# Kernel tuning notes

Measured on AMD Instinct MI355X. Metric: run time of the kernel, lower is better.

The kernel has to match this reference:

```python
import jax, jax.numpy as jnp
import numpy as np

B, C, H, W = 8, 4, 96, 96
HW = H * W
PCT = 95.0            # TRUNCATED_HAUSDORFF_PERCENTILE
IGNORE = 0            # HD_IGNORE_CLASS_INDEX


def setup_inputs() -> dict:
    key = jax.random.key(0)
    k1, k2 = jax.random.split(key)
    predictions = jax.random.normal(k1, (B, C, H, W), dtype=jnp.float32)
    labels = jax.random.randint(k2, (B, H, W), 0, C, dtype=jnp.int32)
    return {"predictions": predictions, "labels": labels}


def _masked_percentile(vals, mask, q):
    """np.percentile(vals[mask], q) with linear interpolation; invalid -> +inf sort to end."""
    n = jnp.sum(mask)
    s = jnp.sort(jnp.where(mask, vals, jnp.inf))
    pos = (q / 100.0) * jnp.maximum(n - 1, 0).astype(vals.dtype)
    lo = jnp.floor(pos).astype(jnp.int32)
    hi = jnp.ceil(pos).astype(jnp.int32)
    frac = pos - lo.astype(vals.dtype)
    return s[lo] * (1.0 - frac) + s[hi] * frac


def _hausdorff(predictions, labels):
    # argmax of softmax == argmax of logits, but keep the softmax for faithfulness
    pred_cls = jnp.argmax(jax.nn.softmax(predictions, axis=1), axis=1)  # [B,H,W]
    cls_ids = jnp.arange(C)
    mask_a = (pred_cls[:, None] == cls_ids[None, :, None, None]).reshape(B * C, HW)  # pred one-hot
    mask_b = (labels[:, None] == cls_ids[None, :, None, None]).reshape(B * C, HW)    # label one-hot

    # Pixel coordinates (row, col) as in np.argwhere; pairwise Euclidean distances once.
    ys, xs = jnp.meshgrid(jnp.arange(H), jnp.arange(W), indexing="ij")
    coords = jnp.stack([ys.ravel(), xs.ravel()], axis=1).astype(jnp.float32)  # [HW,2]
    sq = jnp.sum(coords * coords, axis=1)
    D = jnp.sqrt(jnp.maximum(sq[:, None] + sq[None, :] - 2.0 * (coords @ coords.T), 0.0))  # [HW,HW]

    def per_pair(masks):
        ma, mb = masks  # [HW] bool each
        fwd_min = jnp.min(jnp.where(mb[None, :], D, jnp.inf), axis=1)  # min dist A-pixel -> B set
        rev_min = jnp.min(jnp.where(ma[:, None], D, jnp.inf), axis=0)  # min dist B-pixel -> A set
        f = _masked_percentile(fwd_min, ma, PCT)
        r = _masked_percentile(rev_min, mb, PCT)
        return jnp.stack([f, r, jnp.maximum(f, r)])

    res = jax.lax.map(per_pair, (mask_a, mask_b)).reshape(B, C, 3)
    valid = (jnp.arange(C) != IGNORE)
    per_class = jnp.where(valid[None, :, None], res, 0.0).mean(axis=0)  # [C,3] mean over batch

    def finalize(v):  # v: [C] -> [C+2]: per-class, mean(all), mean(excluding class 0)
        return jnp.concatenate([v, jnp.mean(v)[None], jnp.mean(v[1:])[None]])

    FHD = finalize(per_class[:, 0])
    RHD = finalize(per_class[:, 1])
    MHD = finalize(per_class[:, 2])
    return MHD, FHD, RHD


def reference(predictions, labels):
    return _hausdorff(predictions, labels)
```

## Files before the change

kernel.cpp:

```cpp
#include <hip/hip_runtime.h>
#include <math.h>

#define B_   8
#define C_   4
#define H_   96
#define W_   96
#define HW_  9216
#define NBINS 18052
#define INFBIN 18051
#define NH32 ((NBINS + 1) / 2)
#define NT   1024
#define NBLK 64
#define NW   16

__global__ __launch_bounds__(NT) void hd_main(const float* __restrict__ preds,
                                              const int*   __restrict__ labels,
                                              float* __restrict__ frws)
{
    __shared__ unsigned long long qmask[HW_ / 64];
    __shared__ unsigned long long tmask[HW_ / 64];
    __shared__ unsigned short g2u[HW_];
    __shared__ unsigned int   h32[NH32];
    __shared__ int wsum[NW];
    __shared__ int twv[NW], qwv[NW], zwv[NW], bwv[NW];
    __shared__ int svsel[2];

    const int id  = blockIdx.x;
    const int dir = id & 1;
    const int bc  = id >> 1;
    const int b   = bc >> 2;
    const int c   = bc & 3;
    const int tid = threadIdx.x;
    const int lane = tid & 63;
    const int wid  = tid >> 6;

    const float* Pb = preds  + (size_t)b * C_ * HW_;
    const int*   Lb = labels + (size_t)b * HW_;

    for (int i = tid; i < NH32; i += NT) h32[i] = 0u;
    if (tid == 0) { svsel[0] = -1; svsel[1] = -1; }

    {
        int myT = 0, myQ = 0, myN0 = 0;
        #pragma unroll 3
        for (int k = 0; k < HW_ / NT; ++k) {
            const int p = k * NT + tid;
            float v0 = Pb[p];
            float v1 = Pb[HW_ + p];
            float v2 = Pb[2 * HW_ + p];
            float v3 = Pb[3 * HW_ + p];
            int bi = 0; float bv = v0;
            if (v1 > bv) { bv = v1; bi = 1; }
            if (v2 > bv) { bv = v2; bi = 2; }
            if (v3 > bv) { bv = v3; bi = 3; }
            const int lab = Lb[p];
            const bool pm = (bi == c);
            const bool lm = (lab == c);
            const bool qm = dir ? lm : pm;
            const bool tm = dir ? pm : lm;
            const unsigned long long qb = __ballot(qm);
            const unsigned long long tb = __ballot(tm);
            if (lane == 0) {
                qmask[p >> 6] = qb;
                tmask[p >> 6] = tb;
                myQ  += __popcll(qb);
                myT  += __popcll(tb);
                myN0 += __popcll(qb & tb);
            }
        }
        if (lane == 0) { twv[wid] = myT; qwv[wid] = myQ; zwv[wid] = myN0; }
    }
    __syncthreads();

    int nT = 0;
    #pragma unroll
    for (int w = 0; w < NW; ++w) nT += twv[w];
    const int tEmpty = (nT == 0);

    for (int k = 0; k < HW_ / NT; ++k) {
        const int p = k * NT + tid;
        const int y = p / W_;
        const int x = p - y * W_;
        const int bp = y * W_;
        const int wi = bp >> 6;
        const int sh = bp & 63;
        const unsigned long long w0 = tmask[wi];
        const unsigned long long w1 = tmask[wi + 1];
        unsigned long long A, Bw;
        if (sh == 0) { A = w0;                       Bw = w1 & 0xFFFFFFFFull; }
        else         { A = (w0 >> 32) | (w1 << 32); Bw = w1 >> 32; }

        int dl = 1000, dr = 1000;
        if (x < 64) {
            const unsigned long long ml = A & ((2ull << x) - 1ull);
            if (ml) dl = x - (63 - __builtin_clzll(ml));
            const unsigned long long mr = A & ~((1ull << x) - 1ull);
            if (mr)      dr = __builtin_ctzll(mr) - x;
            else if (Bw) dr = 64 + __builtin_ctzll(Bw) - x;
        } else {
            const int xb = x - 64;
            const unsigned long long ml = Bw & ((2ull << xb) - 1ull);
            if (ml)     dl = x - (64 + 63 - __builtin_clzll(ml));
            else if (A) dl = x - (63 - __builtin_clzll(A));
            const unsigned long long mr = Bw & ~((1ull << xb) - 1ull);
            if (mr) dr = 64 + __builtin_ctzll(mr) - x;
        }
        const int g = min(dl, dr);
        g2u[p] = (g >= 96) ? (unsigned short)40000
                           : (unsigned short)(g * g);
    }
    __syncthreads();

    {
        int bmax = 0;
        if (!tEmpty) {
            for (int k = 0; k < HW_ / NT; ++k) {
                const int p = k * NT + tid;
                const int qbit = (int)((qmask[p >> 6] >> (p & 63)) & 1ull);
                if (!qbit) continue;
                const int tbit = (int)((tmask[p >> 6] >> (p & 63)) & 1ull);
                if (tbit) continue;
                const int y = p / W_;
                const int x = p - y * W_;
                const int a0 = (int)g2u[p];
                const int a1 = (y >= 1)      ? (int)g2u[p - W_]     : 0x7FFF0000;
                const int a2 = (y + 1 < H_)  ? (int)g2u[p + W_]     : 0x7FFF0000;
                const int a3 = (y >= 2)      ? (int)g2u[p - 2 * W_] : 0x7FFF0000;
                const int a4 = (y + 2 < H_)  ? (int)g2u[p + 2 * W_] : 0x7FFF0000;
                int best = min(a0, min(min(a1 + 1, a2 + 1), min(a3 + 4, a4 + 4)));
                for (int off = 3; off < H_; ++off) {
                    const int o2 = off * off;
                    if (o2 >= best) break;
                    const int r1 = y - off;
                    const int r2 = y + off;
                    if (r1 >= 0) best = min(best, o2 + (int)g2u[r1 * W_ + x]);
                    if (r2 < H_) best = min(best, o2 + (int)g2u[r2 * W_ + x]);
                }
                bmax = max(bmax, best);
                atomicAdd(&h32[best >> 1], 1u << ((best & 1) << 4));
            }
        }
        #pragma unroll
        for (int d = 32; d >= 1; d >>= 1) bmax = max(bmax, __shfl_xor(bmax, d, 64));
        if (lane == 0) bwv[wid] = bmax;
    }
    __syncthreads();

    int nQ = 0, n0 = 0, maxd2 = 0;
    #pragma unroll
    for (int w = 0; w < NW; ++w) {
        nQ += qwv[w]; n0 += zwv[w]; maxd2 = max(maxd2, bwv[w]);
    }
    const int h0x = (!tEmpty) ? n0 : 0;
    const int CHUNK = (NBINS + NT - 1) / NT;
    const int base_i = tid * CHUNK;
    int lsum = (base_i == 0) ? h0x : 0;
    for (int j = 0; j < CHUNK; ++j) {
        const int i = base_i + j;
        if (i > maxd2) break;
        lsum += (int)((h32[i >> 1] >> ((i & 1) << 4)) & 0xFFFFu);
    }
    int incl = lsum;
    #pragma unroll
    for (int d = 1; d < 64; d <<= 1) {
        const int t = __shfl_up(incl, d, 64);
        if (lane >= d) incl += t;
    }
    if (lane == 63) wsum[wid] = incl;
    __syncthreads();
    if (wid == 0) {
        const int w = (lane < NW) ? wsum[lane] : 0;
        int wincl = w;
        #pragma unroll
        for (int d = 1; d < NW; d <<= 1) {
            const int t = __shfl_up(wincl, d, 64);
            if (lane >= d) wincl += t;
        }
        if (lane < NW) wsum[lane] = wincl - w;
    }
    __syncthreads();

    int nm1 = nQ - 1; if (nm1 < 0) nm1 = 0;
    const float posf = 0.95f * (float)nm1;
    const int lo = (int)floorf(posf);
    const int hi = (int)ceilf(posf);
    const float frac = posf - (float)lo;

    int run = (incl - lsum) + wsum[wid];
    for (int j = 0; j < CHUNK; ++j) {
        const int i = base_i + j;
        if (i > maxd2) break;
        int h = (int)((h32[i >> 1] >> ((i & 1) << 4)) & 0xFFFFu);
        if (i == 0) h += h0x;
        if (h > 0) {
            const int nrun = run + h;
            if (run <= lo && lo < nrun) svsel[0] = i;
            if (run <= hi && hi < nrun) svsel[1] = i;
            run = nrun;
        }
    }
    __syncthreads();

    if (tid == 0) {
        const int svlo = svsel[0], svhi = svsel[1];
        const float vlo = (svlo < 0) ? __builtin_inff() : (float)sqrt((double)svlo);
        const float vhi = (svhi < 0) ? __builtin_inff() : (float)sqrt((double)svhi);
        frws[id] = vlo * (1.0f - frac) + vhi * frac;
    }
}

__global__ __launch_bounds__(64) void hd_fin(const float* __restrict__ frws,
                                             float* __restrict__ out)
{
    __shared__ float fr[NBLK];
    const int tid = threadIdx.x;
    fr[tid] = frws[tid];
    __syncthreads();
    if (tid == 0) {
        float F[4], R[4], M[4];
        for (int c = 0; c < 4; ++c) {
            if (c == 0) { F[c] = R[c] = M[c] = 0.0f; continue; }
            float sf = 0.0f, sr = 0.0f, sm = 0.0f;
            for (int b = 0; b < 8; ++b) {
                const float f = fr[((b * 4 + c) << 1) + 0];
                const float r = fr[((b * 4 + c) << 1) + 1];
                sf += f; sr += r;
                float m = f > r ? f : r;
                if (f != f || r != r) m = f + r;
                sm += m;
            }
            F[c] = sf / 8.0f; R[c] = sr / 8.0f; M[c] = sm / 8.0f;
        }
        float* o = out;
        o[0] = M[0]; o[1] = M[1]; o[2] = M[2]; o[3] = M[3];
        o[4] = (M[0] + M[1] + M[2] + M[3]) / 4.0f;
        o[5] = (M[1] + M[2] + M[3]) / 3.0f;
        o += 6;
        o[0] = F[0]; o[1] = F[1]; o[2] = F[2]; o[3] = F[3];
        o[4] = (F[0] + F[1] + F[2] + F[3]) / 4.0f;
        o[5] = (F[1] + F[2] + F[3]) / 3.0f;
        o += 6;
        o[0] = R[0]; o[1] = R[1]; o[2] = R[2]; o[3] = R[3];
        o[4] = (R[0] + R[1] + R[2] + R[3]) / 4.0f;
        o[5] = (R[1] + R[2] + R[3]) / 3.0f;
    }
}

extern "C" void kernel_launch(void* const* d_in, const int* in_sizes, int n_in,
                              void* d_out, int out_size, void* d_ws, size_t ws_size,
                              hipStream_t stream)
{
    const float* preds  = (const float*)d_in[0];
    const int*   labels = (const int*)d_in[1];
    float* frws = (float*)d_ws;

    hipLaunchKernelGGL(hd_main, dim3(NBLK), dim3(NT), 0, stream,
                       preds, labels, frws);
    hipLaunchKernelGGL(hd_fin, dim3(1), dim3(64), 0, stream,
                       frws, (float*)d_out);
}
```

Measured before the change: 24.13 us.

## Vectorize mask build with byte masks and single-wave histogram scan

The mask-building loop now has each thread load 8 pixels with float4/int4 vector loads and pack the results into byte-granular shared masks, replacing per-pixel ballots. Counts are reduced with wave shuffles. Row-window extraction reads three 32-bit words per row from the byte masks. The block-wide histogram prefix scan and its two barriers are replaced by a single wave that scans bins in 64-wide chunks up to the max distance, while the other waves exit early. This trades parallel scan width for fewer synchronisations; the serial chunk loop can get long when the max distance is large.

```diff
diff --git a/kernel.cpp b/kernel.cpp
--- a/kernel.cpp
+++ b/kernel.cpp
@@ -7,23 +7,21 @@
 #define W_   96
 #define HW_  9216
 #define NBINS 18052
-#define INFBIN 18051
 #define NH32 ((NBINS + 1) / 2)
 #define NT   1024
 #define NBLK 64
 #define NW   16
+#define NGRP 1152
 
 __global__ __launch_bounds__(NT) void hd_main(const float* __restrict__ preds,
                                               const int*   __restrict__ labels,
                                               float* __restrict__ frws)
 {
-    __shared__ unsigned long long qmask[HW_ / 64];
-    __shared__ unsigned long long tmask[HW_ / 64];
+    __shared__ unsigned char  qmb[NGRP];
+    __shared__ unsigned char  tmb[NGRP];
     __shared__ unsigned short g2u[HW_];
     __shared__ unsigned int   h32[NH32];
-    __shared__ int wsum[NW];
     __shared__ int twv[NW], qwv[NW], zwv[NW], bwv[NW];
-    __shared__ int svsel[2];
 
     const int id  = blockIdx.x;
     const int dir = id & 1;
@@ -38,35 +36,56 @@
     const int*   Lb = labels + (size_t)b * HW_;
 
     for (int i = tid; i < NH32; i += NT) h32[i] = 0u;
-    if (tid == 0) { svsel[0] = -1; svsel[1] = -1; }
 
     {
         int myT = 0, myQ = 0, myN0 = 0;
-        #pragma unroll 3
-        for (int k = 0; k < HW_ / NT; ++k) {
-            const int p = k * NT + tid;
-            float v0 = Pb[p];
-            float v1 = Pb[HW_ + p];
-            float v2 = Pb[2 * HW_ + p];
-            float v3 = Pb[3 * HW_ + p];
-            int bi = 0; float bv = v0;
-            if (v1 > bv) { bv = v1; bi = 1; }
-            if (v2 > bv) { bv = v2; bi = 2; }
-            if (v3 > bv) { bv = v3; bi = 3; }
-            const int lab = Lb[p];
-            const bool pm = (bi == c);
-            const bool lm = (lab == c);
-            const bool qm = dir ? lm : pm;
-            const bool tm = dir ? pm : lm;
-            const unsigned long long qb = __ballot(qm);
-            const unsigned long long tb = __ballot(tm);
-            if (lane == 0) {
-                qmask[p >> 6] = qb;
-                tmask[p >> 6] = tb;
-                myQ  += __popcll(qb);
-                myT  += __popcll(tb);
-                myN0 += __popcll(qb & tb);
-            }
+        #pragma unroll
+        for (int k = 0; k < 2; ++k) {
+            const int g = k * NT + tid;
+            if (g < NGRP) {
+                const int bp = g * 8;
+                const float4 a0 = *(const float4*)(Pb + bp);
+                const float4 b0 = *(const float4*)(Pb + bp + 4);
+                const float4 a1 = *(const float4*)(Pb + HW_ + bp);
+                const float4 b1 = *(const float4*)(Pb + HW_ + bp + 4);
+                const float4 a2 = *(const float4*)(Pb + 2 * HW_ + bp);
+                const float4 b2 = *(const float4*)(Pb + 2 * HW_ + bp + 4);
+                const float4 a3 = *(const float4*)(Pb + 3 * HW_ + bp);
+                const float4 b3 = *(const float4*)(Pb + 3 * HW_ + bp + 4);
+                const int4   l0 = *(const int4*)(Lb + bp);
+                const int4   l1 = *(const int4*)(Lb + bp + 4);
+                unsigned tb = 0, qb = 0;
+                #define PX_(j, e0, e1, e2, e3, lj)                              \
+                {   int bi = 0; float bv = (e0);                                \
+                    if ((e1) > bv) { bv = (e1); bi = 1; }                       \
+                    if ((e2) > bv) { bv = (e2); bi = 2; }                       \
+                    if ((e3) > bv) { bv = (e3); bi = 3; }                       \
+                    const bool pm = (bi == c);                                  \
+                    const bool lm = ((lj) == c);                                \
+                    const bool qm = dir ? lm : pm;                              \
+                    const bool tm = dir ? pm : lm;                              \
+                    tb |= (unsigned)tm << (j); qb |= (unsigned)qm << (j); }
+                PX_(0, a0.x, a1.x, a2.x, a3.x, l0.x)
+                PX_(1, a0.y, a1.y, a2.y, a3.y, l0.y)
+                PX_(2, a0.z, a1.z, a2.z, a3.z, l0.z)
+                PX_(3, a0.w, a1.w, a2.w, a3.w, l0.w)
+                PX_(4, b0.x, b1.x, b2.x, b3.x, l1.x)
+                PX_(5, b0.y, b1.y, b2.y, b3.y, l1.y)
+                PX_(6, b0.z, b1.z, b2.z, b3.z, l1.z)
+                PX_(7, b0.w, b1.w, b2.w, b3.w, l1.w)
+                #undef PX_
+                tmb[g] = (unsigned char)tb;
+                qmb[g] = (unsigned char)qb;
+                myT  += __popc(tb);
+                myQ  += __popc(qb);
+                myN0 += __popc(tb & qb);
+            }
+        }
+        #pragma unroll
+        for (int d = 32; d >= 1; d >>= 1) {
+            myT  += __shfl_xor(myT,  d, 64);
+            myQ  += __shfl_xor(myQ,  d, 64);
+            myN0 += __shfl_xor(myN0, d, 64);
         }
         if (lane == 0) { twv[wid] = myT; qwv[wid] = myQ; zwv[wid] = myN0; }
     }
@@ -81,14 +100,12 @@
         const int p = k * NT + tid;
         const int y = p / W_;
         const int x = p - y * W_;
-        const int bp = y * W_;
-        const int wi = bp >> 6;
-        const int sh = bp & 63;
-        const unsigned long long w0 = tmask[wi];
-        const unsigned long long w1 = tmask[wi + 1];
-        unsigned long long A, Bw;
-        if (sh == 0) { A = w0;                       Bw = w1 & 0xFFFFFFFFull; }
-        else         { A = (w0 >> 32) | (w1 << 32); Bw = w1 >> 32; }
+        const unsigned r0 = *(const unsigned*)(tmb + 12 * y);
+        const unsigned r1 = *(const unsigned*)(tmb + 12 * y + 4);
+        const unsigned r2 = *(const unsigned*)(tmb + 12 * y + 8);
+        const unsigned long long A  = (unsigned long long)r0 |
+                                      ((unsigned long long)r1 << 32);
+        const unsigned long long Bw = r2;
 
         int dl = 1000, dr = 1000;
         if (x < 64) {
@@ -116,17 +133,16 @@
         if (!tEmpty) {
             for (int k = 0; k < HW_ / NT; ++k) {
                 const int p = k * NT + tid;
-                const int qbit = (int)((qmask[p >> 6] >> (p & 63)) & 1ull);
-                if (!qbit) continue;
-                const int tbit = (int)((tmask[p >> 6] >> (p & 63)) & 1ull);
-                if (tbit) continue;
+                const int byi = p >> 3, bsh = p & 7;
+                if (!((qmb[byi] >> bsh) & 1)) continue;
+                if ((tmb[byi] >> bsh) & 1) continue;
                 const int y = p / W_;
                 const int x = p - y * W_;
                 const int a0 = (int)g2u[p];
-                const int a1 = (y >= 1)      ? (int)g2u[p - W_]     : 0x7FFF0000;
-                const int a2 = (y + 1 < H_)  ? (int)g2u[p + W_]     : 0x7FFF0000;
-                const int a3 = (y >= 2)      ? (int)g2u[p - 2 * W_] : 0x7FFF0000;
-                const int a4 = (y + 2 < H_)  ? (int)g2u[p + 2 * W_] : 0x7FFF0000;
+                const int a1 = (y >= 1)     ? (int)g2u[p - W_]     : 0x7FFF0000;
+                const int a2 = (y + 1 < H_) ? (int)g2u[p + W_]     : 0x7FFF0000;
+                const int a3 = (y >= 2)     ? (int)g2u[p - 2 * W_] : 0x7FFF0000;
+                const int a4 = (y + 2 < H_) ? (int)g2u[p + 2 * W_] : 0x7FFF0000;
                 int best = min(a0, min(min(a1 + 1, a2 + 1), min(a3 + 4, a4 + 4)));
                 for (int off = 3; off < H_; ++off) {
                     const int o2 = off * off;
@@ -146,39 +162,14 @@
     }
     __syncthreads();
 
-    int nQ = 0, n0 = 0, maxd2 = 0;
+    if (wid != 0) return;
+
+    int nQ = 0, n0s = 0, maxd2 = 0;
     #pragma unroll
     for (int w = 0; w < NW; ++w) {
-        nQ += qwv[w]; n0 += zwv[w]; maxd2 = max(maxd2, bwv[w]);
-    }
-    const int h0x = (!tEmpty) ? n0 : 0;
-    const int CHUNK = (NBINS + NT - 1) / NT;
-    const int base_i = tid * CHUNK;
-    int lsum = (base_i == 0) ? h0x : 0;
-    for (int j = 0; j < CHUNK; ++j) {
-        const int i = base_i + j;
-        if (i > maxd2) break;
-        lsum += (int)((h32[i >> 1] >> ((i & 1) << 4)) & 0xFFFFu);
-    }
-    int incl = lsum;
-    #pragma unroll
-    for (int d = 1; d < 64; d <<= 1) {
-        const int t = __shfl_up(incl, d, 64);
-        if (lane >= d) incl += t;
-    }
-    if (lane == 63) wsum[wid] = incl;
-    __syncthreads();
-    if (wid == 0) {
-        const int w = (lane < NW) ? wsum[lane] : 0;
-        int wincl = w;
-        #pragma unroll
-        for (int d = 1; d < NW; d <<= 1) {
-            const int t = __shfl_up(wincl, d, 64);
-            if (lane >= d) wincl += t;
-        }
-        if (lane < NW) wsum[lane] = wincl - w;
-    }
-    __syncthreads();
+        nQ += qwv[w]; n0s += zwv[w]; maxd2 = max(maxd2, bwv[w]);
+    }
+    const int h0x = tEmpty ? 0 : n0s;
 
     int nm1 = nQ - 1; if (nm1 < 0) nm1 = 0;
     const float posf = 0.95f * (float)nm1;
@@ -186,23 +177,36 @@
     const int hi = (int)ceilf(posf);
     const float frac = posf - (float)lo;
 
-    int run = (incl - lsum) + wsum[wid];
-    for (int j = 0; j < CHUNK; ++j) {
-        const int i = base_i + j;
-        if (i > maxd2) break;
-        int h = (int)((h32[i >> 1] >> ((i & 1) << 4)) & 0xFFFFu);
-        if (i == 0) h += h0x;
-        if (h > 0) {
-            const int nrun = run + h;
-            if (run <= lo && lo < nrun) svsel[0] = i;
-            if (run <= hi && hi < nrun) svsel[1] = i;
-            run = nrun;
-        }
-    }
-    __syncthreads();
-
-    if (tid == 0) {
-        const int svlo = svsel[0], svhi = svsel[1];
+    int svlo = -1, svhi = -1;
+    if (!tEmpty) {
+        int run = 0;
+        for (int base = 0; base <= maxd2; base += 64) {
+            const int i = base + lane;
+            int h = 0;
+            if (i <= maxd2) {
+                h = (int)((h32[i >> 1] >> ((i & 1) << 4)) & 0xFFFFu);
+                if (i == 0) h += h0x;
+            }
+            int inc = h;
+            #pragma unroll
+            for (int d = 1; d < 64; d <<= 1) {
+                const int t = __shfl_up(inc, d, 64);
+                if (lane >= d) inc += t;
+            }
+            const int excl = run + inc - h;
+            if (h > 0) {
+                if (excl <= lo && lo < excl + h) svlo = i;
+                if (excl <= hi && hi < excl + h) svhi = i;
+            }
+            run += __shfl(inc, 63, 64);
+        }
+        #pragma unroll
+        for (int d = 32; d >= 1; d >>= 1) {
+            svlo = max(svlo, __shfl_xor(svlo, d, 64));
+            svhi = max(svhi, __shfl_xor(svhi, d, 64));
+        }
+    }
+    if (lane == 0) {
         const float vlo = (svlo < 0) ? __builtin_inff() : (float)sqrt((double)svlo);
         const float vhi = (svhi < 0) ? __builtin_inff() : (float)sqrt((double)svhi);
         frws[id] = vlo * (1.0f - frac) + vhi * frac;
```

Result: faster. 20.40 us, median of 2 (-15.4%).
